# Kernel optimization log

Measured on AMD Instinct MI355X. Metric: run time of the kernel, lower is better.

The kernel has to match this reference:

```python
import jax, jax.numpy as jnp
import numpy as np

EPS = 1e-5

def _bn(x, g, b, m, v):
    # inference BatchNorm over last (channel) axis
    return (x - m) * (g * jax.lax.rsqrt(v + EPS)) + b

def setup_inputs() -> dict:
    key = jax.random.key(0)
    ks = jax.random.split(key, 20)
    B, C, H, W, HID = 4, 192, 56, 56, 384
    rn = lambda k, s: jax.random.normal(k, s, dtype=jnp.float32)
    ru = lambda k, s: jax.random.uniform(k, s, dtype=jnp.float32)
    return {
        "x": rn(ks[0], (B, C, H, W)),
        "fc1_w": rn(ks[1], (C, C)) * 0.05, "fc1_b": rn(ks[2], (C,)) * 0.05,
        "bn1_g": ru(ks[3], (C,)), "bn1_b": rn(ks[4], (C,)) * 0.05,
        "bn1_m": rn(ks[5], (C,)) * 0.05, "bn1_v": ru(ks[6], (C,)) + 0.5,
        "gcn_w": rn(ks[7], (HID, 2 * C)) * 0.05, "gcn_b": rn(ks[8], (HID,)) * 0.05,
        "bng_g": ru(ks[9], (HID,)), "bng_b": rn(ks[10], (HID,)) * 0.05,
        "bng_m": rn(ks[11], (HID,)) * 0.05, "bng_v": ru(ks[12], (HID,)) + 0.5,
        "fc2_w": rn(ks[13], (C, HID)) * 0.05, "fc2_b": rn(ks[14], (C,)) * 0.05,
        "bn2_g": ru(ks[15], (C,)), "bn2_b": rn(ks[16], (C,)) * 0.05,
        "bn2_m": rn(ks[17], (C,)) * 0.05, "bn2_v": ru(ks[18], (C,)) + 0.5,
    }

K = 9

def reference(x, fc1_w, fc1_b, bn1_g, bn1_b, bn1_m, bn1_v,
              gcn_w, gcn_b, bng_g, bng_b, bng_m, bng_v,
              fc2_w, fc2_b, bn2_g, bn2_b, bn2_m, bn2_v):
    B, C, H, W = x.shape
    N = H * W
    xf = x.reshape(B, C, N).transpose(0, 2, 1)          # [B, N, C] nodes
    shortcut = xf
    # fc1: conv1x1 + BN
    h = _bn(jnp.einsum('bnc,oc->bno', xf, fc1_w) + fc1_b, bn1_g, bn1_b, bn1_m, bn1_v)
    # dynamic kNN on detached features (negative squared distance, self included)
    hd = jax.lax.stop_gradient(h)
    sq = jnp.sum(hd * hd, axis=-1)                       # [B, N]
    dist = sq[:, :, None] - 2.0 * jnp.einsum('bnc,bmc->bnm', hd, hd) + sq[:, None, :]
    _, idx = jax.lax.top_k(-dist, K)                     # [B, N, K]
    # gather neighbor features
    x_j = jax.vmap(lambda f, i: f[i])(h, idx)            # [B, N, K, C]
    x_i = h[:, :, None, :]
    e = jnp.concatenate([jnp.broadcast_to(x_i, x_j.shape), x_j - x_i], axis=-1)  # [B,N,K,2C]
    m = jnp.einsum('bnkc,oc->bnko', e, gcn_w) + gcn_b    # [B, N, K, HID]
    g = jnp.max(m, axis=2)                               # edge-conv max aggregation
    g = jax.nn.gelu(_bn(g, bng_g, bng_b, bng_m, bng_v), approximate=False)
    # fc2 + residual
    out = _bn(jnp.einsum('bno,co->bnc', g, fc2_w) + fc2_b, bn2_g, bn2_b, bn2_m, bn2_v) + shortcut
    return out.transpose(0, 2, 1).reshape(B, C, H, W)
```

## Files before the change

kernel.cpp:

```cpp
#include <hip/hip_runtime.h>
#include <math.h>

#define N_PIX 3136
#define C_DIM 192
#define HID_DIM 384
#define BATCH 4
#define KNN 9
#define EPS_BN 1e-5f

typedef __attribute__((ext_vector_type(4))) float f32x4;
typedef __attribute__((ext_vector_type(8))) short s16x8;
typedef unsigned short u16;

static const size_t OFF_H   = 0;
static const size_t OFF_SQ  = OFF_H  + (size_t)12544 * 192;
static const size_t OFF_P   = OFF_SQ + 12544;
static const size_t OFF_Q   = OFF_P  + (size_t)12544 * 384;
static const size_t OFF_WC  = OFF_Q  + (size_t)12544 * 384;
static const size_t OFF_CST = OFF_WC + (size_t)768 * 192;
static const size_t OFF_IDX = OFF_CST + 1536;
static const size_t OFF_PL  = OFF_IDX + 112896;

__device__ inline u16 f2bf_rn(float x) {
    unsigned u = __float_as_uint(x);
    unsigned r = u + 0x7fffu + ((u >> 16) & 1u);
    return (u16)(r >> 16);
}

__global__ void k_prep(const float* __restrict__ gcn_w,
                       const float* __restrict__ bn1_g, const float* __restrict__ bn1_b,
                       const float* __restrict__ bn1_m, const float* __restrict__ bn1_v,
                       const float* __restrict__ bng_g, const float* __restrict__ bng_b,
                       const float* __restrict__ bng_m, const float* __restrict__ bng_v,
                       const float* __restrict__ bn2_g, const float* __restrict__ bn2_b,
                       const float* __restrict__ bn2_m, const float* __restrict__ bn2_v,
                       float* __restrict__ wc, float* __restrict__ cst)
{
    int t = blockIdx.x * 256 + threadIdx.x;
    if (t < 768 * 192) {
        int o = t / 192, c = t % 192;
        float v;
        if (o < 384) v = gcn_w[o * 384 + c] - gcn_w[o * 384 + 192 + c];
        else         v = gcn_w[(o - 384) * 384 + 192 + c];
        wc[t] = v;
    }
    int u = t - 768 * 192;
    if (u >= 0 && u < 768) {
        if (u < 192) {
            float s = bn1_g[u] / sqrtf(bn1_v[u] + EPS_BN);
            cst[u] = s; cst[192 + u] = bn1_b[u] - bn1_m[u] * s;
        } else if (u < 576) {
            int ch = u - 192;
            float s = bng_g[ch] / sqrtf(bng_v[ch] + EPS_BN);
            cst[384 + ch] = s; cst[768 + ch] = bng_b[ch] - bng_m[ch] * s;
        } else {
            int ch = u - 576;
            float s = bn2_g[ch] / sqrtf(bn2_v[ch] + EPS_BN);
            cst[1152 + ch] = s; cst[1344 + ch] = bn2_b[ch] - bn2_m[ch] * s;
        }
    }
}

__global__ __launch_bounds__(256) void k1_fc1_bn1(
    const float* __restrict__ x, const float* __restrict__ w,
    const float* __restrict__ bias, const float* __restrict__ cst,
    float* __restrict__ h)
{
    __shared__ float As[32][64];
    __shared__ float Bs[32][64];
    int bx = blockIdx.x;
    int o0 = blockIdx.y * 64;
    int b  = bx / 49;
    int n0 = (bx % 49) * 64;
    const float* xb = x + (size_t)b * C_DIM * N_PIX;
    int t = threadIdx.x;
    int tx = t & 15, ty = t >> 4;
    float acc[4][4] = {};
    for (int kc = 0; kc < 6; ++kc) {
        #pragma unroll
        for (int p = 0; p < 2; ++p) {
            int idx = t + p * 256;
            int kk = idx >> 4, j4 = idx & 15;
            float4 v = *reinterpret_cast<const float4*>(xb + (size_t)(kc * 32 + kk) * N_PIX + n0 + j4 * 4);
            *reinterpret_cast<float4*>(&As[kk][j4 * 4]) = v;
        }
        #pragma unroll
        for (int p = 0; p < 2; ++p) {
            int idx = t + p * 256;
            int oo = idx >> 3, c4 = idx & 7;
            float4 v = *reinterpret_cast<const float4*>(w + (size_t)(o0 + oo) * C_DIM + kc * 32 + c4 * 4);
            Bs[c4 * 4 + 0][oo] = v.x; Bs[c4 * 4 + 1][oo] = v.y;
            Bs[c4 * 4 + 2][oo] = v.z; Bs[c4 * 4 + 3][oo] = v.w;
        }
        __syncthreads();
        #pragma unroll
        for (int kk = 0; kk < 32; ++kk) {
            float4 av = *reinterpret_cast<const float4*>(&As[kk][ty * 4]);
            float4 bv = *reinterpret_cast<const float4*>(&Bs[kk][tx * 4]);
            float a[4] = {av.x, av.y, av.z, av.w};
            float bb[4] = {bv.x, bv.y, bv.z, bv.w};
            #pragma unroll
            for (int i = 0; i < 4; ++i)
                #pragma unroll
                for (int j = 0; j < 4; ++j) acc[i][j] += a[i] * bb[j];
        }
        __syncthreads();
    }
    #pragma unroll
    for (int i = 0; i < 4; ++i) {
        int n = n0 + ty * 4 + i;
        size_t r = (size_t)b * N_PIX + n;
        float vals[4];
        #pragma unroll
        for (int j = 0; j < 4; ++j) {
            int o = o0 + tx * 4 + j;
            vals[j] = (acc[i][j] + bias[o]) * cst[o] + cst[192 + o];
        }
        *reinterpret_cast<float4*>(h + r * C_DIM + o0 + tx * 4) =
            make_float4(vals[0], vals[1], vals[2], vals[3]);
    }
}

__global__ __launch_bounds__(256) void k_sq(const float* __restrict__ h, float* __restrict__ sq)
{
    int r = blockIdx.x * 256 + threadIdx.x;
    const float* hr = h + (size_t)r * C_DIM;
    float s = 0.f;
    #pragma unroll
    for (int c = 0; c < C_DIM; c += 4) {
        float4 v = *reinterpret_cast<const float4*>(hr + c);
        s += v.x * v.x + v.y * v.y + v.z * v.z + v.w * v.w;
    }
    sq[r] = s;
}

__global__ __launch_bounds__(256) void k_split(const float* __restrict__ h, u16* __restrict__ h2)
{
    int t = blockIdx.x * 256 + threadIdx.x;
    int base = t * 4;
    int r = base / C_DIM, c = base % C_DIM;
    float4 v = *reinterpret_cast<const float4*>(h + base);
    float f[4] = {v.x, v.y, v.z, v.w};
    u16 hi[4], lo[4];
    #pragma unroll
    for (int j = 0; j < 4; ++j) {
        hi[j] = f2bf_rn(f[j]);
        float hf = __uint_as_float((unsigned)hi[j] << 16);
        lo[j] = f2bf_rn(f[j] - hf);
    }
    u16* dst = h2 + (size_t)r * 384 + c;
    dst[0] = hi[0]; dst[1] = hi[1]; dst[2] = hi[2]; dst[3] = hi[3];
    dst[192] = lo[0]; dst[193] = lo[1]; dst[194] = lo[2]; dst[195] = lo[3];
}

__global__ __launch_bounds__(256) void k2_pq(
    const float* __restrict__ h, const float* __restrict__ wc,
    const float* __restrict__ gcnb, float* __restrict__ P, float* __restrict__ Q)
{
    __shared__ float As[32][64];
    __shared__ float Bs[32][64];
    int r0 = blockIdx.x * 64;
    int o0 = blockIdx.y * 64;
    int t = threadIdx.x;
    int tx = t & 15, ty = t >> 4;
    float acc[4][4] = {};
    for (int kc = 0; kc < 6; ++kc) {
        #pragma unroll
        for (int p = 0; p < 2; ++p) {
            int idx = t + p * 256;
            int j = idx >> 3, c4 = idx & 7;
            float4 v = *reinterpret_cast<const float4*>(h + (size_t)(r0 + j) * C_DIM + kc * 32 + c4 * 4);
            As[c4 * 4 + 0][j] = v.x; As[c4 * 4 + 1][j] = v.y;
            As[c4 * 4 + 2][j] = v.z; As[c4 * 4 + 3][j] = v.w;
        }
        #pragma unroll
        for (int p = 0; p < 2; ++p) {
            int idx = t + p * 256;
            int oo = idx >> 3, c4 = idx & 7;
            float4 v = *reinterpret_cast<const float4*>(wc + (size_t)(o0 + oo) * C_DIM + kc * 32 + c4 * 4);
            Bs[c4 * 4 + 0][oo] = v.x; Bs[c4 * 4 + 1][oo] = v.y;
            Bs[c4 * 4 + 2][oo] = v.z; Bs[c4 * 4 + 3][oo] = v.w;
        }
        __syncthreads();
        #pragma unroll
        for (int kk = 0; kk < 32; ++kk) {
            float4 av = *reinterpret_cast<const float4*>(&As[kk][ty * 4]);
            float4 bv = *reinterpret_cast<const float4*>(&Bs[kk][tx * 4]);
            float a[4] = {av.x, av.y, av.z, av.w};
            float bb[4] = {bv.x, bv.y, bv.z, bv.w};
            #pragma unroll
            for (int i = 0; i < 4; ++i)
                #pragma unroll
                for (int j = 0; j < 4; ++j) acc[i][j] += a[i] * bb[j];
        }
        __syncthreads();
    }
    bool isP = (o0 < HID_DIM);
    #pragma unroll
    for (int i = 0; i < 4; ++i) {
        size_t r = (size_t)(r0 + ty * 4 + i);
        int ocb = o0 + tx * 4;
        float vals[4];
        #pragma unroll
        for (int j = 0; j < 4; ++j)
            vals[j] = acc[i][j] + (isP ? gcnb[ocb + j] : 0.0f);
        float4 vv = make_float4(vals[0], vals[1], vals[2], vals[3]);
        if (isP) *reinterpret_cast<float4*>(P + r * HID_DIM + ocb) = vv;
        else     *reinterpret_cast<float4*>(Q + r * HID_DIM + (ocb - HID_DIM)) = vv;
    }
}

#define B_STRIDE 392
__global__ __launch_bounds__(256) void k3_knn(
    const u16* __restrict__ h2, const float* __restrict__ sq,
    unsigned long long* __restrict__ pl)
{
    __shared__ u16 Bs[64 * B_STRIDE];
    int bx    = blockIdx.x;
    int b     = bx / 343;
    int rem   = bx % 343;
    int strip = rem / 7;
    int mc    = rem % 7;
    int n0 = strip * 64;
    const u16*  hb  = h2 + (size_t)b * N_PIX * 384;
    const float* sqb = sq + (size_t)b * N_PIX;
    int t = threadIdx.x;
    int lane = t & 63, w = t >> 6;
    int col16 = lane & 15, g = lane >> 4;

    s16x8 a_hi[6], a_lo[6];
    {
        const u16* ar = hb + (size_t)(n0 + w * 16 + col16) * 384;
        #pragma unroll
        for (int ko = 0; ko < 6; ++ko) {
            a_hi[ko] = *reinterpret_cast<const s16x8*>(ar + ko * 32 + g * 8);
            a_lo[ko] = *reinterpret_cast<const s16x8*>(ar + 192 + ko * 32 + g * 8);
        }
    }

    unsigned long long cand[4][KNN];
    #pragma unroll
    for (int i = 0; i < 4; ++i)
        #pragma unroll
        for (int q = 0; q < KNN; ++q) cand[i][q] = ~0ull;
    float sqn[4];
    #pragma unroll
    for (int i = 0; i < 4; ++i) sqn[i] = sqb[n0 + w * 16 + g * 4 + i];

    for (int step = 0; step < 7; ++step) {
        int m0 = mc * 448 + step * 64;
        __syncthreads();
        {
            int row = t >> 2, part = t & 3;
            const u16* src = hb + (size_t)(m0 + row) * 384 + part * 8;
            u16* dst = Bs + row * B_STRIDE + part * 8;
            #pragma unroll
            for (int c = 0; c < 12; ++c)
                *reinterpret_cast<s16x8*>(dst + c * 32) =
                    *reinterpret_cast<const s16x8*>(src + c * 32);
        }
        __syncthreads();

        f32x4 acc[4];
        #pragma unroll
        for (int mq = 0; mq < 4; ++mq) acc[mq] = (f32x4){0.f, 0.f, 0.f, 0.f};
        #pragma unroll
        for (int ko = 0; ko < 6; ++ko) {
            #pragma unroll
            for (int mq = 0; mq < 4; ++mq) {
                const u16* bp = Bs + (mq * 16 + col16) * B_STRIDE + ko * 32 + g * 8;
                s16x8 bhi = *reinterpret_cast<const s16x8*>(bp);
                s16x8 blo = *reinterpret_cast<const s16x8*>(bp + 192);
                acc[mq] = __builtin_amdgcn_mfma_f32_16x16x32_bf16(a_hi[ko], bhi, acc[mq], 0, 0, 0);
                acc[mq] = __builtin_amdgcn_mfma_f32_16x16x32_bf16(a_hi[ko], blo, acc[mq], 0, 0, 0);
                acc[mq] = __builtin_amdgcn_mfma_f32_16x16x32_bf16(a_lo[ko], bhi, acc[mq], 0, 0, 0);
            }
        }

        #pragma unroll
        for (int mq = 0; mq < 4; ++mq) {
            int m = m0 + mq * 16 + col16;
            float sqm = sqb[m];
            #pragma unroll
            for (int i = 0; i < 4; ++i) {
                float dist = (sqn[i] - 2.0f * acc[mq][i]) + sqm;
                unsigned u = __float_as_uint(dist);
                u = (u & 0x80000000u) ? ~u : (u | 0x80000000u);
                unsigned long long key = ((unsigned long long)u << 32) | (unsigned)m;
                if (key < cand[i][KNN - 1]) {
                    cand[i][KNN - 1] = key;
                    #pragma unroll
                    for (int q = KNN - 1; q > 0; --q) {
                        unsigned long long lo = cand[i][q - 1], hi = cand[i][q];
                        if (hi < lo) { cand[i][q - 1] = hi; cand[i][q] = lo; }
                    }
                }
            }
        }
    }

    #pragma unroll
    for (int i = 0; i < 4; ++i) {
        int n = n0 + w * 16 + g * 4 + i;
        size_t rowg = (size_t)b * N_PIX + n;
        for (int r = 0; r < KNN; ++r) {
            unsigned long long my = cand[i][0];
            unsigned long long gm = my;
            #pragma unroll
            for (int s = 1; s < 16; s <<= 1) {
                unsigned long long o = __shfl_xor(gm, s);
                if (o < gm) gm = o;
            }
            if (gm == my) {
                #pragma unroll
                for (int q = 0; q < KNN - 1; ++q) cand[i][q] = cand[i][q + 1];
                cand[i][KNN - 1] = ~0ull;
            }
            if (col16 == 0)
                pl[(rowg * 7 + mc) * KNN + r] = gm;
        }
    }
}

__global__ __launch_bounds__(256) void k3b_merge(
    const unsigned long long* __restrict__ pl, int* __restrict__ idxout)
{
    int r = blockIdx.x * 256 + threadIdx.x;
    const unsigned long long* base = pl + (size_t)r * 63;
    unsigned long long list[KNN];
    #pragma unroll
    for (int q = 0; q < KNN; ++q) list[q] = ~0ull;
    for (int c = 0; c < 63; ++c) {
        unsigned long long k = base[c];
        if (k < list[KNN - 1]) {
            list[KNN - 1] = k;
            #pragma unroll
            for (int q = KNN - 1; q > 0; --q) {
                unsigned long long lo = list[q - 1], hi = list[q];
                if (hi < lo) { list[q - 1] = hi; list[q] = lo; }
            }
        }
    }
    #pragma unroll
    for (int q = 0; q < KNN; ++q)
        idxout[(size_t)r * KNN + q] = (int)(list[q] & 0xffffffffu);
}

__global__ __launch_bounds__(384) void k4_agg(
    float* __restrict__ P, const float* __restrict__ Q,
    const int* __restrict__ idx, const float* __restrict__ cst)
{
    int blk = blockIdx.x;
    int b = blk / N_PIX;
    size_t row = (size_t)blk;
    const int* id = idx + row * KNN;
    int o = threadIdx.x;
    const float* Qb = Q + (size_t)b * N_PIX * HID_DIM;
    float v = -INFINITY;
    #pragma unroll
    for (int k = 0; k < KNN; ++k)
        v = fmaxf(v, Qb[(size_t)id[k] * HID_DIM + o]);
    float gp = P[row * HID_DIM + o] + v;
    float y = gp * cst[384 + o] + cst[768 + o];
    float ge = 0.5f * y * (1.0f + erff(y * 0.70710678118654752f));
    P[row * HID_DIM + o] = ge;
}

__global__ __launch_bounds__(256) void k5_fc2_bn2(
    const float* __restrict__ g, const float* __restrict__ w,
    const float* __restrict__ bias, const float* __restrict__ cst,
    const float* __restrict__ x, float* __restrict__ out)
{
    __shared__ float As[32][64];
    __shared__ float Bs[32][64];
    int bx = blockIdx.x;
    int c0 = blockIdx.y * 64;
    int b  = bx / 49;
    int n0 = (bx % 49) * 64;
    int r0 = bx * 64;
    int t = threadIdx.x;
    int tx = t & 15, ty = t >> 4;
    float acc[4][4] = {};
    for (int kc = 0; kc < 12; ++kc) {
        #pragma unroll
        for (int p = 0; p < 2; ++p) {
            int idx = t + p * 256;
            int j = idx >> 3, c4 = idx & 7;
            float4 v = *reinterpret_cast<const float4*>(g + (size_t)(r0 + j) * HID_DIM + kc * 32 + c4 * 4);
            As[c4 * 4 + 0][j] = v.x; As[c4 * 4 + 1][j] = v.y;
            As[c4 * 4 + 2][j] = v.z; As[c4 * 4 + 3][j] = v.w;
        }
        #pragma unroll
        for (int p = 0; p < 2; ++p) {
            int idx = t + p * 256;
            int oo = idx >> 3, c4 = idx & 7;
            float4 v = *reinterpret_cast<const float4*>(w + (size_t)(c0 + oo) * HID_DIM + kc * 32 + c4 * 4);
            Bs[c4 * 4 + 0][oo] = v.x; Bs[c4 * 4 + 1][oo] = v.y;
            Bs[c4 * 4 + 2][oo] = v.z; Bs[c4 * 4 + 3][oo] = v.w;
        }
        __syncthreads();
        #pragma unroll
        for (int kk = 0; kk < 32; ++kk) {
            float4 av = *reinterpret_cast<const float4*>(&As[kk][ty * 4]);
            float4 bv = *reinterpret_cast<const float4*>(&Bs[kk][tx * 4]);
            float a[4] = {av.x, av.y, av.z, av.w};
            float bb[4] = {bv.x, bv.y, bv.z, bv.w};
            #pragma unroll
            for (int i = 0; i < 4; ++i)
                #pragma unroll
                for (int j = 0; j < 4; ++j) acc[i][j] += a[i] * bb[j];
        }
        __syncthreads();
    }
    #pragma unroll
    for (int i = 0; i < 4; ++i) {
        int n = n0 + ty * 4 + i;
        #pragma unroll
        for (int j = 0; j < 4; ++j) {
            int c = c0 + tx * 4 + j;
            size_t a = (size_t)b * C_DIM * N_PIX + (size_t)c * N_PIX + n;
            float y = (acc[i][j] + bias[c]) * cst[1152 + c] + cst[1344 + c] + x[a];
            out[a] = y;
        }
    }
}

extern "C" void kernel_launch(void* const* d_in, const int* in_sizes, int n_in,
                              void* d_out, int out_size, void* d_ws, size_t ws_size,
                              hipStream_t stream)
{
    const float* x      = (const float*)d_in[0];
    const float* fc1_w  = (const float*)d_in[1];
    const float* fc1_b  = (const float*)d_in[2];
    const float* bn1_g  = (const float*)d_in[3];
    const float* bn1_b  = (const float*)d_in[4];
    const float* bn1_m  = (const float*)d_in[5];
    const float* bn1_v  = (const float*)d_in[6];
    const float* gcn_w  = (const float*)d_in[7];
    const float* gcn_b  = (const float*)d_in[8];
    const float* bng_g  = (const float*)d_in[9];
    const float* bng_b  = (const float*)d_in[10];
    const float* bng_m  = (const float*)d_in[11];
    const float* bng_v  = (const float*)d_in[12];
    const float* fc2_w  = (const float*)d_in[13];
    const float* fc2_b  = (const float*)d_in[14];
    const float* bn2_g  = (const float*)d_in[15];
    const float* bn2_b  = (const float*)d_in[16];
    const float* bn2_m  = (const float*)d_in[17];
    const float* bn2_v  = (const float*)d_in[18];
    float* out = (float*)d_out;

    float* ws  = (float*)d_ws;
    float* h   = ws + OFF_H;
    float* sq  = ws + OFF_SQ;
    float* P   = ws + OFF_P;
    float* Q   = ws + OFF_Q;
    float* wc  = ws + OFF_WC;
    float* cst = ws + OFF_CST;
    int*   idx = (int*)(ws + OFF_IDX);
    unsigned long long* pl = (unsigned long long*)(ws + OFF_PL);
    u16*   h2  = (u16*)(ws + OFF_P);

    k_prep<<<579, 256, 0, stream>>>(gcn_w, bn1_g, bn1_b, bn1_m, bn1_v,
                                    bng_g, bng_b, bng_m, bng_v,
                                    bn2_g, bn2_b, bn2_m, bn2_v, wc, cst);
    k1_fc1_bn1<<<dim3(196, 3), 256, 0, stream>>>(x, fc1_w, fc1_b, cst, h);
    k_sq<<<49, 256, 0, stream>>>(h, sq);
    k_split<<<2352, 256, 0, stream>>>(h, h2);
    k3_knn<<<1372, 256, 0, stream>>>(h2, sq, pl);
    k3b_merge<<<49, 256, 0, stream>>>(pl, idx);
    k2_pq<<<dim3(196, 12), 256, 0, stream>>>(h, wc, gcn_b, P, Q);
    k4_agg<<<12544, 384, 0, stream>>>(P, Q, idx, cst);
    k5_fc2_bn2<<<dim3(196, 3), 256, 0, stream>>>(P, fc2_w, fc2_b, cst, x, out);
}
```

Measured before the change: 464.4 us.

## Move PQ and fc2 GEMMs to split-bf16 MFMA and drop LDS staging in kNN

Replaces the FP32 scalar LDS-tiled GEMMs in k2_pq and k5_fc2_bn2 with MFMA bf16 GEMMs. These use a hi/lo bf16 split to keep near-FP32 accuracy, with the weights pre-split in k_prep. P and Q are stored as bf16 to halve gather traffic in k4_agg, which now writes its output as a hi/lo bf16 pair. The kNN kernel stops staging B tiles in shared memory and loads them straight from global into registers in 32-column steps. Storing P/Q in plain bf16 lowers precision, and dropping LDS in kNN relies on cache hits.

```diff
diff --git a/kernel.cpp b/kernel.cpp
--- a/kernel.cpp
+++ b/kernel.cpp
@@ -4,7 +4,6 @@
 #define N_PIX 3136
 #define C_DIM 192
 #define HID_DIM 384
-#define BATCH 4
 #define KNN 9
 #define EPS_BN 1e-5f
 
@@ -13,39 +12,53 @@
 typedef unsigned short u16;
 
 static const size_t OFF_H   = 0;
-static const size_t OFF_SQ  = OFF_H  + (size_t)12544 * 192;
-static const size_t OFF_P   = OFF_SQ + 12544;
-static const size_t OFF_Q   = OFF_P  + (size_t)12544 * 384;
-static const size_t OFF_WC  = OFF_Q  + (size_t)12544 * 384;
-static const size_t OFF_CST = OFF_WC + (size_t)768 * 192;
-static const size_t OFF_IDX = OFF_CST + 1536;
-static const size_t OFF_PL  = OFF_IDX + 112896;
+static const size_t OFF_SQ  = 2408448;
+static const size_t OFF_H2  = 2420992;
+static const size_t OFF_G2  = 0;
+static const size_t OFF_PBF = 4829440;
+static const size_t OFF_QBF = 7237888;
+static const size_t OFF_WC2 = 9646336;
+static const size_t OFF_W5  = 9793792;
+static const size_t OFF_CST = 9867520;
+static const size_t OFF_IDX = 9869056;
+static const size_t OFF_PL  = 9981952;
 
 __device__ inline u16 f2bf_rn(float x) {
     unsigned u = __float_as_uint(x);
     unsigned r = u + 0x7fffu + ((u >> 16) & 1u);
     return (u16)(r >> 16);
 }
-
-__global__ void k_prep(const float* __restrict__ gcn_w,
+__device__ inline float bf2f(u16 v) { return __uint_as_float((unsigned)v << 16); }
+__device__ inline void split2(float x, u16& hi, u16& lo) {
+    hi = f2bf_rn(x);
+    lo = f2bf_rn(x - bf2f(hi));
+}
+
+__global__ void k_prep(const float* __restrict__ gcn_w, const float* __restrict__ fc2_w,
                        const float* __restrict__ bn1_g, const float* __restrict__ bn1_b,
                        const float* __restrict__ bn1_m, const float* __restrict__ bn1_v,
                        const float* __restrict__ bng_g, const float* __restrict__ bng_b,
                        const float* __restrict__ bng_m, const float* __restrict__ bng_v,
                        const float* __restrict__ bn2_g, const float* __restrict__ bn2_b,
                        const float* __restrict__ bn2_m, const float* __restrict__ bn2_v,
-                       float* __restrict__ wc, float* __restrict__ cst)
+                       u16* __restrict__ wc2, u16* __restrict__ w5, float* __restrict__ cst)
 {
     int t = blockIdx.x * 256 + threadIdx.x;
     if (t < 768 * 192) {
         int o = t / 192, c = t % 192;
-        float v;
-        if (o < 384) v = gcn_w[o * 384 + c] - gcn_w[o * 384 + 192 + c];
-        else         v = gcn_w[(o - 384) * 384 + 192 + c];
-        wc[t] = v;
-    }
-    int u = t - 768 * 192;
-    if (u >= 0 && u < 768) {
+        float v = (o < 384) ? gcn_w[o * 384 + c] - gcn_w[o * 384 + 192 + c]
+                            : gcn_w[(o - 384) * 384 + 192 + c];
+        u16 hi, lo; split2(v, hi, lo);
+        wc2[(size_t)o * 384 + c] = hi;
+        wc2[(size_t)o * 384 + 192 + c] = lo;
+    } else if (t < 768 * 192 + 192 * 384) {
+        int u = t - 768 * 192;
+        int c = u / 384, k = u % 384;
+        u16 hi, lo; split2(fc2_w[(size_t)c * 384 + k], hi, lo);
+        w5[(size_t)c * 768 + k] = hi;
+        w5[(size_t)c * 768 + 384 + k] = lo;
+    } else if (t < 768 * 192 + 192 * 384 + 768) {
+        int u = t - 768 * 192 - 192 * 384;
         if (u < 192) {
             float s = bn1_g[u] / sqrtf(bn1_v[u] + EPS_BN);
             cst[u] = s; cst[192 + u] = bn1_b[u] - bn1_m[u] * s;
@@ -141,81 +154,18 @@
     int r = base / C_DIM, c = base % C_DIM;
     float4 v = *reinterpret_cast<const float4*>(h + base);
     float f[4] = {v.x, v.y, v.z, v.w};
-    u16 hi[4], lo[4];
+    u16* dst = h2 + (size_t)r * 384 + c;
     #pragma unroll
     for (int j = 0; j < 4; ++j) {
-        hi[j] = f2bf_rn(f[j]);
-        float hf = __uint_as_float((unsigned)hi[j] << 16);
-        lo[j] = f2bf_rn(f[j] - hf);
-    }
-    u16* dst = h2 + (size_t)r * 384 + c;
-    dst[0] = hi[0]; dst[1] = hi[1]; dst[2] = hi[2]; dst[3] = hi[3];
-    dst[192] = lo[0]; dst[193] = lo[1]; dst[194] = lo[2]; dst[195] = lo[3];
-}
-
-__global__ __launch_bounds__(256) void k2_pq(
-    const float* __restrict__ h, const float* __restrict__ wc,
-    const float* __restrict__ gcnb, float* __restrict__ P, float* __restrict__ Q)
-{
-    __shared__ float As[32][64];
-    __shared__ float Bs[32][64];
-    int r0 = blockIdx.x * 64;
-    int o0 = blockIdx.y * 64;
-    int t = threadIdx.x;
-    int tx = t & 15, ty = t >> 4;
-    float acc[4][4] = {};
-    for (int kc = 0; kc < 6; ++kc) {
-        #pragma unroll
-        for (int p = 0; p < 2; ++p) {
-            int idx = t + p * 256;
-            int j = idx >> 3, c4 = idx & 7;
-            float4 v = *reinterpret_cast<const float4*>(h + (size_t)(r0 + j) * C_DIM + kc * 32 + c4 * 4);
-            As[c4 * 4 + 0][j] = v.x; As[c4 * 4 + 1][j] = v.y;
-            As[c4 * 4 + 2][j] = v.z; As[c4 * 4 + 3][j] = v.w;
-        }
-        #pragma unroll
-        for (int p = 0; p < 2; ++p) {
-            int idx = t + p * 256;
-            int oo = idx >> 3, c4 = idx & 7;
-            float4 v = *reinterpret_cast<const float4*>(wc + (size_t)(o0 + oo) * C_DIM + kc * 32 + c4 * 4);
-            Bs[c4 * 4 + 0][oo] = v.x; Bs[c4 * 4 + 1][oo] = v.y;
-            Bs[c4 * 4 + 2][oo] = v.z; Bs[c4 * 4 + 3][oo] = v.w;
-        }
-        __syncthreads();
-        #pragma unroll
-        for (int kk = 0; kk < 32; ++kk) {
-            float4 av = *reinterpret_cast<const float4*>(&As[kk][ty * 4]);
-            float4 bv = *reinterpret_cast<const float4*>(&Bs[kk][tx * 4]);
-            float a[4] = {av.x, av.y, av.z, av.w};
-            float bb[4] = {bv.x, bv.y, bv.z, bv.w};
-            #pragma unroll
-            for (int i = 0; i < 4; ++i)
-                #pragma unroll
-                for (int j = 0; j < 4; ++j) acc[i][j] += a[i] * bb[j];
-        }
-        __syncthreads();
-    }
-    bool isP = (o0 < HID_DIM);
-    #pragma unroll
-    for (int i = 0; i < 4; ++i) {
-        size_t r = (size_t)(r0 + ty * 4 + i);
-        int ocb = o0 + tx * 4;
-        float vals[4];
-        #pragma unroll
-        for (int j = 0; j < 4; ++j)
-            vals[j] = acc[i][j] + (isP ? gcnb[ocb + j] : 0.0f);
-        float4 vv = make_float4(vals[0], vals[1], vals[2], vals[3]);
-        if (isP) *reinterpret_cast<float4*>(P + r * HID_DIM + ocb) = vv;
-        else     *reinterpret_cast<float4*>(Q + r * HID_DIM + (ocb - HID_DIM)) = vv;
-    }
-}
-
-#define B_STRIDE 392
+        u16 hi, lo; split2(f[j], hi, lo);
+        dst[j] = hi; dst[192 + j] = lo;
+    }
+}
+
 __global__ __launch_bounds__(256) void k3_knn(
     const u16* __restrict__ h2, const float* __restrict__ sq,
     unsigned long long* __restrict__ pl)
 {
-    __shared__ u16 Bs[64 * B_STRIDE];
     int bx    = blockIdx.x;
     int b     = bx / 343;
     int rem   = bx % 343;
@@ -247,43 +197,34 @@
     #pragma unroll
     for (int i = 0; i < 4; ++i) sqn[i] = sqb[n0 + w * 16 + g * 4 + i];
 
-    for (int step = 0; step < 7; ++step) {
-        int m0 = mc * 448 + step * 64;
-        __syncthreads();
-        {
-            int row = t >> 2, part = t & 3;
-            const u16* src = hb + (size_t)(m0 + row) * 384 + part * 8;
-            u16* dst = Bs + row * B_STRIDE + part * 8;
-            #pragma unroll
-            for (int c = 0; c < 12; ++c)
-                *reinterpret_cast<s16x8*>(dst + c * 32) =
-                    *reinterpret_cast<const s16x8*>(src + c * 32);
-        }
-        __syncthreads();
-
-        f32x4 acc[4];
-        #pragma unroll
-        for (int mq = 0; mq < 4; ++mq) acc[mq] = (f32x4){0.f, 0.f, 0.f, 0.f};
+    for (int step = 0; step < 14; ++step) {
+        int m0 = mc * 448 + step * 32;
+        const u16* bb = hb + (size_t)(m0 + col16) * 384 + g * 8;
+        f32x4 acc0 = {0.f, 0.f, 0.f, 0.f};
+        f32x4 acc1 = {0.f, 0.f, 0.f, 0.f};
         #pragma unroll
         for (int ko = 0; ko < 6; ++ko) {
-            #pragma unroll
-            for (int mq = 0; mq < 4; ++mq) {
-                const u16* bp = Bs + (mq * 16 + col16) * B_STRIDE + ko * 32 + g * 8;
-                s16x8 bhi = *reinterpret_cast<const s16x8*>(bp);
-                s16x8 blo = *reinterpret_cast<const s16x8*>(bp + 192);
-                acc[mq] = __builtin_amdgcn_mfma_f32_16x16x32_bf16(a_hi[ko], bhi, acc[mq], 0, 0, 0);
-                acc[mq] = __builtin_amdgcn_mfma_f32_16x16x32_bf16(a_hi[ko], blo, acc[mq], 0, 0, 0);
-                acc[mq] = __builtin_amdgcn_mfma_f32_16x16x32_bf16(a_lo[ko], bhi, acc[mq], 0, 0, 0);
-            }
-        }
-
-        #pragma unroll
-        for (int mq = 0; mq < 4; ++mq) {
+            s16x8 b0h = *reinterpret_cast<const s16x8*>(bb + ko * 32);
+            s16x8 b0l = *reinterpret_cast<const s16x8*>(bb + 192 + ko * 32);
+            s16x8 b1h = *reinterpret_cast<const s16x8*>(bb + 16 * 384 + ko * 32);
+            s16x8 b1l = *reinterpret_cast<const s16x8*>(bb + 16 * 384 + 192 + ko * 32);
+            acc0 = __builtin_amdgcn_mfma_f32_16x16x32_bf16(a_hi[ko], b0h, acc0, 0, 0, 0);
+            acc0 = __builtin_amdgcn_mfma_f32_16x16x32_bf16(a_hi[ko], b0l, acc0, 0, 0, 0);
+            acc0 = __builtin_amdgcn_mfma_f32_16x16x32_bf16(a_lo[ko], b0h, acc0, 0, 0, 0);
+            acc1 = __builtin_amdgcn_mfma_f32_16x16x32_bf16(a_hi[ko], b1h, acc1, 0, 0, 0);
+            acc1 = __builtin_amdgcn_mfma_f32_16x16x32_bf16(a_hi[ko], b1l, acc1, 0, 0, 0);
+            acc1 = __builtin_amdgcn_mfma_f32_16x16x32_bf16(a_lo[ko], b1h, acc1, 0, 0, 0);
+        }
+        float sqm0 = sqb[m0 + col16];
+        float sqm1 = sqb[m0 + 16 + col16];
+        #pragma unroll
+        for (int mq = 0; mq < 2; ++mq) {
             int m = m0 + mq * 16 + col16;
-            float sqm = sqb[m];
+            float sqm = mq ? sqm1 : sqm0;
             #pragma unroll
             for (int i = 0; i < 4; ++i) {
-                float dist = (sqn[i] - 2.0f * acc[mq][i]) + sqm;
+                float dot = mq ? acc1[i] : acc0[i];
+                float dist = (sqn[i] - 2.0f * dot) + sqm;
                 unsigned u = __float_as_uint(dist);
                 u = (u & 0x80000000u) ? ~u : (u | 0x80000000u);
                 unsigned long long key = ((unsigned long long)u << 32) | (unsigned)m;
@@ -346,81 +287,129 @@
         idxout[(size_t)r * KNN + q] = (int)(list[q] & 0xffffffffu);
 }
 
+__global__ __launch_bounds__(256) void k2_pq(
+    const u16* __restrict__ h2, const u16* __restrict__ wc2,
+    const float* __restrict__ gcnb, u16* __restrict__ Pbf, u16* __restrict__ Qbf)
+{
+    int r0 = blockIdx.x * 64;
+    int o0 = blockIdx.y * 32;
+    int t = threadIdx.x, lane = t & 63, w = t >> 6;
+    int col16 = lane & 15, g = lane >> 4;
+
+    s16x8 a_hi[6], a_lo[6];
+    {
+        const u16* ar = h2 + (size_t)(r0 + w * 16 + col16) * 384;
+        #pragma unroll
+        for (int ko = 0; ko < 6; ++ko) {
+            a_hi[ko] = *reinterpret_cast<const s16x8*>(ar + ko * 32 + g * 8);
+            a_lo[ko] = *reinterpret_cast<const s16x8*>(ar + 192 + ko * 32 + g * 8);
+        }
+    }
+    const u16* br = wc2 + (size_t)(o0 + col16) * 384 + g * 8;
+    f32x4 acc0 = {0.f, 0.f, 0.f, 0.f};
+    f32x4 acc1 = {0.f, 0.f, 0.f, 0.f};
+    #pragma unroll
+    for (int ko = 0; ko < 6; ++ko) {
+        s16x8 b0h = *reinterpret_cast<const s16x8*>(br + ko * 32);
+        s16x8 b0l = *reinterpret_cast<const s16x8*>(br + 192 + ko * 32);
+        s16x8 b1h = *reinterpret_cast<const s16x8*>(br + 16 * 384 + ko * 32);
+        s16x8 b1l = *reinterpret_cast<const s16x8*>(br + 16 * 384 + 192 + ko * 32);
+        acc0 = __builtin_amdgcn_mfma_f32_16x16x32_bf16(a_hi[ko], b0h, acc0, 0, 0, 0);
+        acc0 = __builtin_amdgcn_mfma_f32_16x16x32_bf16(a_hi[ko], b0l, acc0, 0, 0, 0);
+        acc0 = __builtin_amdgcn_mfma_f32_16x16x32_bf16(a_lo[ko], b0h, acc0, 0, 0, 0);
+        acc1 = __builtin_amdgcn_mfma_f32_16x16x32_bf16(a_hi[ko], b1h, acc1, 0, 0, 0);
+        acc1 = __builtin_amdgcn_mfma_f32_16x16x32_bf16(a_hi[ko], b1l, acc1, 0, 0, 0);
+        acc1 = __builtin_amdgcn_mfma_f32_16x16x32_bf16(a_lo[ko], b1h, acc1, 0, 0, 0);
+    }
+    bool isP = (o0 < HID_DIM);
+    #pragma unroll
+    for (int oq = 0; oq < 2; ++oq) {
+        int o = o0 + oq * 16 + col16;
+        float bias = isP ? gcnb[o] : 0.0f;
+        #pragma unroll
+        for (int i = 0; i < 4; ++i) {
+            size_t r = (size_t)(r0 + w * 16 + g * 4 + i);
+            float v = (oq ? acc1[i] : acc0[i]) + bias;
+            u16 bv = f2bf_rn(v);
+            if (isP) Pbf[r * 384 + o] = bv;
+            else     Qbf[r * 384 + (o - HID_DIM)] = bv;
+        }
+    }
+}
+
 __global__ __launch_bounds__(384) void k4_agg(
-    float* __restrict__ P, const float* __restrict__ Q,
-    const int* __restrict__ idx, const float* __restrict__ cst)
+    const u16* __restrict__ Pbf, const u16* __restrict__ Qbf,
+    const int* __restrict__ idx, const float* __restrict__ cst,
+    u16* __restrict__ g2)
 {
     int blk = blockIdx.x;
     int b = blk / N_PIX;
     size_t row = (size_t)blk;
     const int* id = idx + row * KNN;
     int o = threadIdx.x;
-    const float* Qb = Q + (size_t)b * N_PIX * HID_DIM;
+    const u16* Qb = Qbf + (size_t)b * N_PIX * 384;
     float v = -INFINITY;
     #pragma unroll
     for (int k = 0; k < KNN; ++k)
-        v = fmaxf(v, Qb[(size_t)id[k] * HID_DIM + o]);
-    float gp = P[row * HID_DIM + o] + v;
-    float y = gp * cst[384 + o] + cst[768 + o];
+        v = fmaxf(v, bf2f(Qb[(size_t)id[k] * 384 + o]));
+    float p = bf2f(Pbf[row * 384 + o]);
+    float y = (p + v) * cst[384 + o] + cst[768 + o];
     float ge = 0.5f * y * (1.0f + erff(y * 0.70710678118654752f));
-    P[row * HID_DIM + o] = ge;
+    u16 hi, lo; split2(ge, hi, lo);
+    g2[row * 768 + o] = hi;
+    g2[row * 768 + 384 + o] = lo;
 }
 
 __global__ __launch_bounds__(256) void k5_fc2_bn2(
-    const float* __restrict__ g, const float* __restrict__ w,
-    const float* __restrict__ bias, const float* __restrict__ cst,
+    const u16* __restrict__ g2, const u16* __restrict__ w5,
+    const float* __restrict__ fc2b, const float* __restrict__ cst,
     const float* __restrict__ x, float* __restrict__ out)
 {
-    __shared__ float As[32][64];
-    __shared__ float Bs[32][64];
     int bx = blockIdx.x;
-    int c0 = blockIdx.y * 64;
+    int c0 = blockIdx.y * 32;
     int b  = bx / 49;
     int n0 = (bx % 49) * 64;
     int r0 = bx * 64;
-    int t = threadIdx.x;
-    int tx = t & 15, ty = t >> 4;
-    float acc[4][4] = {};
-    for (int kc = 0; kc < 12; ++kc) {
-        #pragma unroll
-        for (int p = 0; p < 2; ++p) {
-            int idx = t + p * 256;
-            int j = idx >> 3, c4 = idx & 7;
-            float4 v = *reinterpret_cast<const float4*>(g + (size_t)(r0 + j) * HID_DIM + kc * 32 + c4 * 4);
-            As[c4 * 4 + 0][j] = v.x; As[c4 * 4 + 1][j] = v.y;
-            As[c4 * 4 + 2][j] = v.z; As[c4 * 4 + 3][j] = v.w;
-        }
-        #pragma unroll
-        for (int p = 0; p < 2; ++p) {
-            int idx = t + p * 256;
-            int oo = idx >> 3, c4 = idx & 7;
-            float4 v = *reinterpret_cast<const float4*>(w + (size_t)(c0 + oo) * HID_DIM + kc * 32 + c4 * 4);
-            Bs[c4 * 4 + 0][oo] = v.x; Bs[c4 * 4 + 1][oo] = v.y;
-            Bs[c4 * 4 + 2][oo] = v.z; Bs[c4 * 4 + 3][oo] = v.w;
-        }
-        __syncthreads();
-        #pragma unroll
-        for (int kk = 0; kk < 32; ++kk) {
-            float4 av = *reinterpret_cast<const float4*>(&As[kk][ty * 4]);
-            float4 bv = *reinterpret_cast<const float4*>(&Bs[kk][tx * 4]);
-            float a[4] = {av.x, av.y, av.z, av.w};
-            float bb[4] = {bv.x, bv.y, bv.z, bv.w};
-            #pragma unroll
-            for (int i = 0; i < 4; ++i)
-                #pragma unroll
-                for (int j = 0; j < 4; ++j) acc[i][j] += a[i] * bb[j];
-        }
-        __syncthreads();
-    }
-    #pragma unroll
-    for (int i = 0; i < 4; ++i) {
-        int n = n0 + ty * 4 + i;
-        #pragma unroll
-        for (int j = 0; j < 4; ++j) {
-            int c = c0 + tx * 4 + j;
+    int t = threadIdx.x, lane = t & 63, w = t >> 6;
+    int col16 = lane & 15, g = lane >> 4;
+
+    const u16* ar = g2 + (size_t)(r0 + w * 16 + col16) * 768;
+    const u16* br = w5 + (size_t)(c0 + col16) * 768 + g * 8;
+    f32x4 acc0 = {0.f, 0.f, 0.f, 0.f};
+    f32x4 acc1 = {0.f, 0.f, 0.f, 0.f};
+    #pragma unroll
+    for (int kh = 0; kh < 2; ++kh) {
+        s16x8 a_hi[6], a_lo[6];
+        #pragma unroll
+        for (int ko = 0; ko < 6; ++ko) {
+            a_hi[ko] = *reinterpret_cast<const s16x8*>(ar + (kh * 6 + ko) * 32 + g * 8);
+            a_lo[ko] = *reinterpret_cast<const s16x8*>(ar + 384 + (kh * 6 + ko) * 32 + g * 8);
+        }
+        #pragma unroll
+        for (int ko = 0; ko < 6; ++ko) {
+            int kk = (kh * 6 + ko) * 32;
+            s16x8 b0h = *reinterpret_cast<const s16x8*>(br + kk);
+            s16x8 b0l = *reinterpret_cast<const s16x8*>(br + 384 + kk);
+            s16x8 b1h = *reinterpret_cast<const s16x8*>(br + 16 * 768 + kk);
+            s16x8 b1l = *reinterpret_cast<const s16x8*>(br + 16 * 768 + 384 + kk);
+            acc0 = __builtin_amdgcn_mfma_f32_16x16x32_bf16(a_hi[ko], b0h, acc0, 0, 0, 0);
+            acc0 = __builtin_amdgcn_mfma_f32_16x16x32_bf16(a_hi[ko], b0l, acc0, 0, 0, 0);
+            acc0 = __builtin_amdgcn_mfma_f32_16x16x32_bf16(a_lo[ko], b0h, acc0, 0, 0, 0);
+            acc1 = __builtin_amdgcn_mfma_f32_16x16x32_bf16(a_hi[ko], b1h, acc1, 0, 0, 0);
+            acc1 = __builtin_amdgcn_mfma_f32_16x16x32_bf16(a_hi[ko], b1l, acc1, 0, 0, 0);
+            acc1 = __builtin_amdgcn_mfma_f32_16x16x32_bf16(a_lo[ko], b1h, acc1, 0, 0, 0);
+        }
+    }
+    #pragma unroll
+    for (int oq = 0; oq < 2; ++oq) {
+        int c = c0 + oq * 16 + col16;
+        float s2 = cst[1152 + c], sh2 = cst[1344 + c], bz = fc2b[c];
+        #pragma unroll
+        for (int i = 0; i < 4; ++i) {
+            int n = n0 + w * 16 + g * 4 + i;
             size_t a = (size_t)b * C_DIM * N_PIX + (size_t)c * N_PIX + n;
-            float y = (acc[i][j] + bias[c]) * cst[1152 + c] + cst[1344 + c] + x[a];
-            out[a] = y;
+            float v = (oq ? acc1[i] : acc0[i]) + bz;
+            out[a] = v * s2 + sh2 + x[a];
         }
     }
 }
@@ -453,23 +442,26 @@
     float* ws  = (float*)d_ws;
     float* h   = ws + OFF_H;
     float* sq  = ws + OFF_SQ;
-    float* P   = ws + OFF_P;
-    float* Q   = ws + OFF_Q;
-    float* wc  = ws + OFF_WC;
+    u16*   h2  = (u16*)(ws + OFF_H2);
+    u16*   g2  = (u16*)(ws + OFF_G2);
+    u16*   Pbf = (u16*)(ws + OFF_PBF);
+    u16*   Qbf = (u16*)(ws + OFF_QBF);
+    u16*   wc2 = (u16*)(ws + OFF_WC2);
+    u16*   w5  = (u16*)(ws + OFF_W5);
     float* cst = ws + OFF_CST;
     int*   idx = (int*)(ws + OFF_IDX);
     unsigned long long* pl = (unsigned long long*)(ws + OFF_PL);
-    u16*   h2  = (u16*)(ws + OFF_P);
-
-    k_prep<<<579, 256, 0, stream>>>(gcn_w, bn1_g, bn1_b, bn1_m, bn1_v,
+
+    k_prep<<<867, 256, 0, stream>>>(gcn_w, fc2_w,
+                                    bn1_g, bn1_b, bn1_m, bn1_v,
                                     bng_g, bng_b, bng_m, bng_v,
-                                    bn2_g, bn2_b, bn2_m, bn2_v, wc, cst);
+                                    bn2_g, bn2_b, bn2_m, bn2_v, wc2, w5, cst);
     k1_fc1_bn1<<<dim3(196, 3), 256, 0, stream>>>(x, fc1_w, fc1_b, cst, h);
     k_sq<<<49, 256, 0, stream>>>(h, sq);
     k_split<<<2352, 256, 0, stream>>>(h, h2);
     k3_knn<<<1372, 256, 0, stream>>>(h2, sq, pl);
     k3b_merge<<<49, 256, 0, stream>>>(pl, idx);
-    k2_pq<<<dim3(196, 12), 256, 0, stream>>>(h, wc, gcn_b, P, Q);
-    k4_agg<<<12544, 384, 0, stream>>>(P, Q, idx, cst);
-    k5_fc2_bn2<<<dim3(196, 3), 256, 0, stream>>>(P, fc2_w, fc2_b, cst, x, out);
-}
+    k2_pq<<<dim3(196, 24), 256, 0, stream>>>(h2, wc2, gcn_b, Pbf, Qbf);
+    k4_agg<<<12544, 384, 0, stream>>>(Pbf, Qbf, idx, cst, g2);
+    k5_fc2_bn2<<<dim3(196, 6), 256, 0, stream>>>(g2, w5, fc2_b, cst, x, out);
+}
```

New measurement: 537.4 us. 1.16x slower.
